# Kernel optimization log

Measured on AMD Instinct MI355X. Metric: run time of the kernel, lower is better.

Reference implementation:

```python
import jax, jax.numpy as jnp
import numpy as np
import math

B, T, N, D = 2, 2048, 16, 128


def setup_inputs() -> dict:
    key = jax.random.key(0)
    ks = jax.random.split(key, 9)
    s = 1.0 / math.sqrt(D)
    return {
        "x": jax.random.normal(ks[0], (B, T, N, D), dtype=jnp.float32),
        "wq": jax.random.normal(ks[1], (D, D), dtype=jnp.float32) * s,
        "bq": jax.random.normal(ks[2], (D,), dtype=jnp.float32) * 0.02,
        "wk": jax.random.normal(ks[3], (D, D), dtype=jnp.float32) * s,
        "bk": jax.random.normal(ks[4], (D,), dtype=jnp.float32) * 0.02,
        "wv": jax.random.normal(ks[5], (D, D), dtype=jnp.float32) * s,
        "bv": jax.random.normal(ks[6], (D,), dtype=jnp.float32) * 0.02,
        "wp": jax.random.normal(ks[7], (D, D), dtype=jnp.float32) * s,
        "bp": jax.random.normal(ks[8], (D,), dtype=jnp.float32) * 0.02,
    }


def reference(x, wq, bq, wk, bk, wv, bv, wp, bp):
    # x: (B, T, N, D); per-head Linear projections (torch y = x @ W.T + b)
    d = x.shape[-1]
    q = jnp.einsum("btnd,ed->btne", x, wq) + bq  # (B,T,N,D)
    k = jnp.einsum("btnd,ed->btne", x, wk) + bk
    v = jnp.einsum("btnd,ed->btne", x, wv) + bv
    scale = 1.0 / jnp.sqrt(jnp.asarray(d, dtype=x.dtype))
    # scores: (B, N, T, T)
    scores = jnp.einsum("btnd,bsnd->bnts", q, k) * scale
    t = scores.shape[-1]
    causal = jnp.tril(jnp.ones((t, t), dtype=bool))  # (T,T)
    scores = jnp.where(causal[None, None], scores, jnp.asarray(-jnp.inf, scores.dtype))
    w = jax.nn.softmax(scores, axis=-1)
    att = jnp.einsum("bnts,bsnd->btnd", w, v)  # (B,T,N,D)
    out = jnp.einsum("btnd,ed->btne", att, wp) + bp
    return out
```

## Files before the change

### kernel.cpp

```cpp
#include <hip/hip_runtime.h>
#include <cmath>

#define BB 2
#define TT 2048
#define NN 16
#define DD 128
#define NROWS (BB*TT*NN)
#define PLANE (TT*DD)
#define KP 132
#define VP 68

typedef unsigned short u16;
typedef unsigned int   u32;
typedef __attribute__((ext_vector_type(8)))  short s8v;
typedef __attribute__((ext_vector_type(16))) float vf16;

__device__ u16 g_Q [(size_t)NROWS * DD];
__device__ u16 g_K [(size_t)NROWS * DD];
__device__ u16 g_V [(size_t)NROWS * DD];
__device__ u16 g_VT[(size_t)NROWS * DD];

__device__ __forceinline__ u16 f2bf(float f) {
    return (u16)((__float_as_uint(f) + 0x8000u) >> 16);
}
__device__ __forceinline__ u32 pk2(float a, float b) {
    return ((__float_as_uint(a) + 0x8000u) >> 16)
         | ((__float_as_uint(b) + 0x8000u) & 0xFFFF0000u);
}
__device__ __forceinline__ void st8(u16* p, const float4& a, const float4& b) {
    uint2 lo, hi;
    lo.x = pk2(a.x, a.y); lo.y = pk2(a.z, a.w);
    hi.x = pk2(b.x, b.y); hi.y = pk2(b.z, b.w);
    *(uint2*)p       = lo;
    *(uint2*)(p + 4) = hi;
}
__device__ __forceinline__ s8v ld8(const u16* p) {
    short4 a = *(const short4*)p;
    short4 b = *(const short4*)(p + 4);
    return (s8v){a.x, a.y, a.z, a.w, b.x, b.y, b.z, b.w};
}

__global__ __launch_bounds__(256)
void qkv_proj_kernel(const float* __restrict__ x,
                     const float* __restrict__ Wq, const float* __restrict__ Bq,
                     const float* __restrict__ Wk, const float* __restrict__ Bk,
                     const float* __restrict__ Wv, const float* __restrict__ Bv)
{
    __shared__ u16 Xs[128*KP];
    __shared__ u16 Ws[128*KP];

    const int t  = threadIdx.x;
    const int r0 = blockIdx.x * 128;
    const float4* xsrc = (const float4*)(x + (size_t)r0*DD);

    #pragma unroll
    for (int it = 0; it < 8; ++it) {
        int i = t + 256*it;
        int e = i >> 4, c8 = i & 15;
        st8(&Xs[e*KP + c8*8], xsrc[2*i], xsrc[2*i + 1]);
    }
    #pragma unroll
    for (int it = 0; it < 8; ++it) {
        int i = t + 256*it;
        int e = i >> 4, c8 = i & 15;
        st8(&Ws[e*KP + c8*8], ((const float4*)Wq)[2*i], ((const float4*)Wq)[2*i + 1]);
    }
    __syncthreads();

    const int w   = t >> 6;
    const int l31 = t & 31;
    const int q2  = (t >> 5) & 1;

    s8v af[8];
    #pragma unroll
    for (int s = 0; s < 8; ++s)
        af[s] = ld8(&Xs[(w*32 + l31)*KP + s*16 + q2*8]);

    #pragma unroll
    for (int wsel = 0; wsel < 3; ++wsel) {
        const float* Bi = (wsel == 0) ? Bq : (wsel == 1) ? Bk : Bv;
        u16*         Ot = (wsel == 0) ? g_Q : (wsel == 1) ? g_K : g_V;

        vf16 acc[4];
        #pragma unroll
        for (int et = 0; et < 4; ++et)
            #pragma unroll
            for (int i = 0; i < 16; ++i) acc[et][i] = 0.f;

        #pragma unroll
        for (int s = 0; s < 8; ++s) {
            #pragma unroll
            for (int et = 0; et < 4; ++et) {
                s8v bf = ld8(&Ws[(et*32 + l31)*KP + s*16 + q2*8]);
                acc[et] = __builtin_amdgcn_mfma_f32_32x32x16_bf16(af[s], bf, acc[et], 0, 0, 0);
            }
        }

        float bb[4];
        #pragma unroll
        for (int et = 0; et < 4; ++et) bb[et] = Bi[et*32 + l31];

        #pragma unroll
        for (int r = 0; r < 16; ++r) {
            int rl = (r & 3) + 8*(r >> 2) + 4*q2;
            int rg = r0 + w*32 + rl;
            int b = rg >> 15, rem = rg & 32767;
            int tt = rem >> 4, n = rem & 15;
            size_t orow = (size_t)((b*NN + n)*TT + tt) * DD;
            #pragma unroll
            for (int et = 0; et < 4; ++et)
                Ot[orow + et*32 + l31] = f2bf(acc[et][r] + bb[et]);
        }

        if (wsel < 2) {
            const float* Wn = (wsel == 0) ? Wk : Wv;
            __syncthreads();
            #pragma unroll
            for (int it = 0; it < 8; ++it) {
                int i = t + 256*it;
                int e = i >> 4, c8 = i & 15;
                st8(&Ws[e*KP + c8*8], ((const float4*)Wn)[2*i], ((const float4*)Wn)[2*i + 1]);
            }
            __syncthreads();
        }
    }
}

__global__ __launch_bounds__(256)
void out_proj_kernel(const float* __restrict__ W, const float* __restrict__ Bi,
                     float* __restrict__ out)
{
    __shared__ u16 Ws[128*KP];

    const int t  = threadIdx.x;
    const int r0 = blockIdx.x * 128;

    #pragma unroll
    for (int it = 0; it < 8; ++it) {
        int i = t + 256*it;
        int e = i >> 4, c8 = i & 15;
        st8(&Ws[e*KP + c8*8], ((const float4*)W)[2*i], ((const float4*)W)[2*i + 1]);
    }

    const int w   = t >> 6;
    const int l31 = t & 31;
    const int q2  = (t >> 5) & 1;

    s8v af[8];
    {
        const u16* src = g_Q + (size_t)(r0 + w*32 + l31)*DD;
        #pragma unroll
        for (int s = 0; s < 8; ++s)
            af[s] = *(const s8v*)&src[s*16 + q2*8];
    }
    __syncthreads();

    vf16 acc[4];
    #pragma unroll
    for (int et = 0; et < 4; ++et)
        #pragma unroll
        for (int i = 0; i < 16; ++i) acc[et][i] = 0.f;

    #pragma unroll
    for (int s = 0; s < 8; ++s) {
        #pragma unroll
        for (int et = 0; et < 4; ++et) {
            s8v bf = ld8(&Ws[(et*32 + l31)*KP + s*16 + q2*8]);
            acc[et] = __builtin_amdgcn_mfma_f32_32x32x16_bf16(af[s], bf, acc[et], 0, 0, 0);
        }
    }

    float bb[4];
    #pragma unroll
    for (int et = 0; et < 4; ++et) bb[et] = Bi[et*32 + l31];

    #pragma unroll
    for (int r = 0; r < 16; ++r) {
        int rl = (r & 3) + 8*(r >> 2) + 4*q2;
        int rg = r0 + w*32 + rl;
        int b = rg >> 15, rem = rg & 32767;
        int n = rem >> 11, tt = rem & 2047;
        size_t orow = (size_t)((b*TT + tt)*NN + n) * DD;
        #pragma unroll
        for (int et = 0; et < 4; ++et)
            out[orow + et*32 + l31] = acc[et][r] + bb[et];
    }
}

__global__ __launch_bounds__(256)
void vtrans_kernel()
{
    const int t   = threadIdx.x;
    const int blk = blockIdx.x;
    const int pl  = blk >> 7;
    const int seg = blk & 127;
    const size_t plane = (size_t)pl * PLANE;
    const int w = t >> 6, lane = t & 63;
    const int d   = (w & 1)*64 + lane;
    const int tt0 = seg*16 + (w >> 1)*8;

    const u16* src = g_V + plane + (size_t)tt0*DD + d;
    u16 e[8];
    #pragma unroll
    for (int i = 0; i < 8; ++i) e[i] = src[(size_t)i*DD];
    uint4 pk;
    pk.x = (u32)e[0] | ((u32)e[1] << 16);
    pk.y = (u32)e[2] | ((u32)e[3] << 16);
    pk.z = (u32)e[4] | ((u32)e[5] << 16);
    pk.w = (u32)e[6] | ((u32)e[7] << 16);
    *(uint4*)&g_VT[plane + (size_t)d*TT + tt0] = pk;
}

__global__ __launch_bounds__(256, 2)
void attn_kernel()
{
    __shared__ u16 Ks[64*KP];
    __shared__ u16 Vt[128*VP];

    const int t   = threadIdx.x;
    const int grp = blockIdx.x >> 5;
    const int bn  = blockIdx.x & 31;
    const int qt  = (grp < 8) ? (15 - grp) : (grp - 8);
    const int q0  = qt * 128;
    const size_t plane = (size_t)bn * PLANE;
    const u16* Kg = g_K  + plane;
    const u16* Vg = g_VT + plane;

    const int w      = t >> 6;
    const int lane   = t & 63;
    const int lane31 = lane & 31;
    const int q2     = lane >> 5;
    const int qband  = q0 + 32*w;
    const int qrow   = qband + lane31;

    s8v qf[8];
    {
        const u16* Qg = g_Q + plane + (size_t)qrow * DD;
        #pragma unroll
        for (int s = 0; s < 8; ++s)
            qf[s] = *(const s8v*)&Qg[s*16 + q2*8];
    }

    vf16 accO[4];
    #pragma unroll
    for (int dt = 0; dt < 4; ++dt)
        #pragma unroll
        for (int i = 0; i < 16; ++i) accO[dt][i] = 0.f;

    float mrow = -INFINITY, lrow = 0.f;
    const float sc2 = 0.08838834764831845f * 1.4426950408889634f;

    const int nkt = 2*qt + 2;

    uint4 pk[4], pv[4];
    #pragma unroll
    for (int c = 0; c < 4; ++c) {
        int j = t + 256*c;
        int kr = j >> 4, kc = j & 15;
        pk[c] = *(const uint4*)&Kg[kr*DD + kc*8];
        int vr = j >> 3, vc = j & 7;
        pv[c] = *(const uint4*)&Vg[(size_t)vr*TT + vc*8];
    }

    for (int kt = 0; kt < nkt; ++kt) {
        const int k0 = kt*64;
        __syncthreads();
        #pragma unroll
        for (int c = 0; c < 4; ++c) {
            int j = t + 256*c;
            int kr = j >> 4, kc = j & 15;
            uint2 a, b;
            a.x = pk[c].x; a.y = pk[c].y; b.x = pk[c].z; b.y = pk[c].w;
            *(uint2*)&Ks[kr*KP + kc*8]     = a;
            *(uint2*)&Ks[kr*KP + kc*8 + 4] = b;
            int vr = j >> 3, vc = j & 7;
            a.x = pv[c].x; a.y = pv[c].y; b.x = pv[c].z; b.y = pv[c].w;
            *(uint2*)&Vt[vr*VP + vc*8]     = a;
            *(uint2*)&Vt[vr*VP + vc*8 + 4] = b;
        }
        __syncthreads();

        if (kt + 1 < nkt) {
            const u16* Kg2 = Kg + (size_t)(k0 + 64)*DD;
            const u16* Vg2 = Vg + (k0 + 64);
            #pragma unroll
            for (int c = 0; c < 4; ++c) {
                int j = t + 256*c;
                int kr = j >> 4, kc = j & 15;
                pk[c] = *(const uint4*)&Kg2[kr*DD + kc*8];
                int vr = j >> 3, vc = j & 7;
                pv[c] = *(const uint4*)&Vg2[(size_t)vr*TT + vc*8];
            }
        }

        if (k0 > qband + 31) continue;

        vf16 accS[2];
        #pragma unroll
        for (int kk = 0; kk < 2; ++kk)
            #pragma unroll
            for (int i = 0; i < 16; ++i) accS[kk][i] = 0.f;
        #pragma unroll
        for (int s = 0; s < 8; ++s) {
            #pragma unroll
            for (int kk = 0; kk < 2; ++kk) {
                s8v a = ld8(&Ks[(kk*32 + lane31)*KP + s*16 + q2*8]);
                accS[kk] = __builtin_amdgcn_mfma_f32_32x32x16_bf16(a, qf[s], accS[kk], 0, 0, 0);
            }
        }

        float p[2][16];
        const bool tail = (k0 + 63 > qband);
        #pragma unroll
        for (int kk = 0; kk < 2; ++kk)
            #pragma unroll
            for (int r = 0; r < 16; ++r) {
                float sv = accS[kk][r] * sc2;
                if (tail) {
                    int keyg = k0 + kk*32 + (r & 3) + 8*(r >> 2) + 4*q2;
                    if (keyg > qrow) sv = -INFINITY;
                }
                p[kk][r] = sv;
            }

        float vmax = -INFINITY;
        #pragma unroll
        for (int kk = 0; kk < 2; ++kk)
            #pragma unroll
            for (int r = 0; r < 16; ++r) vmax = fmaxf(vmax, p[kk][r]);
        vmax = fmaxf(vmax, __shfl_xor(vmax, 32));
        float mold = mrow;
        float mnew = fmaxf(mold, vmax);
        float alpha = __builtin_amdgcn_exp2f(mold - mnew);
        mrow = mnew;
        float ls = 0.f;
        #pragma unroll
        for (int kk = 0; kk < 2; ++kk)
            #pragma unroll
            for (int r = 0; r < 16; ++r) {
                float e = __builtin_amdgcn_exp2f(p[kk][r] - mnew);
                p[kk][r] = e;
                ls += e;
            }
        ls += __shfl_xor(ls, 32);
        lrow = lrow*alpha + ls;

        if (__any(mnew > mold)) {
            float ar[16];
            #pragma unroll
            for (int r = 0; r < 16; ++r)
                ar[r] = __shfl(alpha, (r & 3) + 8*(r >> 2) + 4*q2);
            #pragma unroll
            for (int dt = 0; dt < 4; ++dt)
                #pragma unroll
                for (int r = 0; r < 16; ++r) accO[dt][r] *= ar[r];
        }

        s8v pf[4];
        #pragma unroll
        for (int tau = 0; tau < 4; ++tau) {
            int kk = tau >> 1, rb = (tau & 1)*8;
            s8v v;
            #pragma unroll
            for (int j = 0; j < 8; ++j)
                v[j] = (short)(__float_as_uint(p[kk][rb + j]) >> 16);
            pf[tau] = v;
        }

        #pragma unroll
        for (int dt = 0; dt < 4; ++dt) {
            const u16* vp = &Vt[(dt*32 + lane31)*VP];
            #pragma unroll
            for (int tau = 0; tau < 4; ++tau) {
                const u16* q = vp + 16*tau + 4*q2;
                short4 lo = *(const short4*)q;
                short4 hi = *(const short4*)(q + 8);
                s8v bvv = {lo.x, lo.y, lo.z, lo.w, hi.x, hi.y, hi.z, hi.w};
                accO[dt] = __builtin_amdgcn_mfma_f32_32x32x16_bf16(pf[tau], bvv, accO[dt], 0, 0, 0);
            }
        }
    }

    float inv = 1.0f / lrow;
    #pragma unroll
    for (int r = 0; r < 16; ++r) {
        int rl = (r & 3) + 8*(r >> 2) + 4*q2;
        float ir = __shfl(inv, rl);
        u16* op = g_Q + plane + (size_t)(qband + rl)*DD;
        #pragma unroll
        for (int dt = 0; dt < 4; ++dt)
            op[dt*32 + lane31] = f2bf(accO[dt][r] * ir);
    }
}

extern "C" void kernel_launch(void* const* d_in, const int* in_sizes, int n_in,
                              void* d_out, int out_size, void* d_ws, size_t ws_size,
                              hipStream_t stream)
{
    const float* x  = (const float*)d_in[0];
    const float* wq = (const float*)d_in[1];
    const float* bq = (const float*)d_in[2];
    const float* wk = (const float*)d_in[3];
    const float* bk = (const float*)d_in[4];
    const float* wv = (const float*)d_in[5];
    const float* bv = (const float*)d_in[6];
    const float* wp = (const float*)d_in[7];
    const float* bp = (const float*)d_in[8];
    float* out = (float*)d_out;
    (void)d_ws; (void)ws_size;

    dim3 blk(256);
    qkv_proj_kernel<<<dim3(NROWS/128), blk, 0, stream>>>(
        x, wq, bq, wk, bk, wv, bv);
    vtrans_kernel<<<dim3(BB*NN*128), blk, 0, stream>>>();
    attn_kernel<<<dim3(BB*NN*(TT/128)), blk, 0, stream>>>();
    out_proj_kernel<<<dim3(NROWS/128), blk, 0, stream>>>(wp, bp, out);
}
```

Baseline: 204.9 us.

## Shrink attention blocks to 64 queries, fold softmax scale into Q, lazy rescale

The attention kernel now uses 128-thread blocks covering 64 query rows, doubling the grid and removing the per-wave skip of masked tiles, with a new causal load-balancing order. The softmax scale and log2e are folded into Q at projection time. The online softmax now rescales only when the running max grows by more than 8, which saves multiplies but risks accumulator range growth. MFMA sections get raised wave priority, and the V transpose goes through shared memory so global reads are coalesced. Each thread also now holds twice as many prefetch registers.

New measurement: 198.9 us. 1.03x faster.

```diff
diff --git a/kernel.cpp b/kernel.cpp
--- a/kernel.cpp
+++ b/kernel.cpp
@@ -108,8 +108,11 @@
             int tt = rem >> 4, n = rem & 15;
             size_t orow = (size_t)((b*NN + n)*TT + tt) * DD;
             #pragma unroll
-            for (int et = 0; et < 4; ++et)
-                Ot[orow + et*32 + l31] = f2bf(acc[et][r] + bb[et]);
+            for (int et = 0; et < 4; ++et) {
+                float ov = acc[et][r] + bb[et];
+                if (wsel == 0) ov *= 0.12752053685940512f;
+                Ot[orow + et*32 + l31] = f2bf(ov);
+            }
         }
 
         if (wsel < 2) {
@@ -190,28 +193,39 @@
 __global__ __launch_bounds__(256)
 void vtrans_kernel()
 {
+    __shared__ u16 L[64*KP];
+
     const int t   = threadIdx.x;
     const int blk = blockIdx.x;
-    const int pl  = blk >> 7;
-    const int seg = blk & 127;
+    const int pl  = blk >> 5;
+    const int tt0 = (blk & 31) * 64;
     const size_t plane = (size_t)pl * PLANE;
-    const int w = t >> 6, lane = t & 63;
-    const int d   = (w & 1)*64 + lane;
-    const int tt0 = seg*16 + (w >> 1)*8;
-
-    const u16* src = g_V + plane + (size_t)tt0*DD + d;
-    u16 e[8];
-    #pragma unroll
-    for (int i = 0; i < 8; ++i) e[i] = src[(size_t)i*DD];
-    uint4 pk;
-    pk.x = (u32)e[0] | ((u32)e[1] << 16);
-    pk.y = (u32)e[2] | ((u32)e[3] << 16);
-    pk.z = (u32)e[4] | ((u32)e[5] << 16);
-    pk.w = (u32)e[6] | ((u32)e[7] << 16);
-    *(uint4*)&g_VT[plane + (size_t)d*TT + tt0] = pk;
-}
-
-__global__ __launch_bounds__(256, 2)
+
+    #pragma unroll
+    for (int c = 0; c < 4; ++c) {
+        int j = t + 256*c;
+        int row = j >> 4, c16 = j & 15;
+        uint4 v = *(const uint4*)&g_V[plane + (size_t)(tt0 + row)*DD + c16*8];
+        *(uint4*)&L[row*KP + c16*8] = v;
+    }
+    __syncthreads();
+    #pragma unroll
+    for (int c = 0; c < 4; ++c) {
+        int j = t + 256*c;
+        int d = j >> 3, tc = j & 7;
+        u16 e[8];
+        #pragma unroll
+        for (int i = 0; i < 8; ++i) e[i] = L[(tc*8 + i)*KP + d];
+        uint4 pkv;
+        pkv.x = (u32)e[0] | ((u32)e[1] << 16);
+        pkv.y = (u32)e[2] | ((u32)e[3] << 16);
+        pkv.z = (u32)e[4] | ((u32)e[5] << 16);
+        pkv.w = (u32)e[6] | ((u32)e[7] << 16);
+        *(uint4*)&g_VT[plane + (size_t)d*TT + tt0 + tc*8] = pkv;
+    }
+}
+
+__global__ __launch_bounds__(128, 2)
 void attn_kernel()
 {
     __shared__ u16 Ks[64*KP];
@@ -220,8 +234,12 @@
     const int t   = threadIdx.x;
     const int grp = blockIdx.x >> 5;
     const int bn  = blockIdx.x & 31;
-    const int qt  = (grp < 8) ? (15 - grp) : (grp - 8);
-    const int q0  = qt * 128;
+    int qt;
+    if      (grp < 8)  qt = 31 - grp;
+    else if (grp < 16) qt = grp - 8;
+    else if (grp < 24) qt = 39 - grp;
+    else               qt = grp - 16;
+
     const size_t plane = (size_t)bn * PLANE;
     const u16* Kg = g_K  + plane;
     const u16* Vg = g_VT + plane;
@@ -230,7 +248,7 @@
     const int lane   = t & 63;
     const int lane31 = lane & 31;
     const int q2     = lane >> 5;
-    const int qband  = q0 + 32*w;
+    const int qband  = qt*64 + 32*w;
     const int qrow   = qband + lane31;
 
     s8v qf[8];
@@ -248,14 +266,13 @@
         for (int i = 0; i < 16; ++i) accO[dt][i] = 0.f;
 
     float mrow = -INFINITY, lrow = 0.f;
-    const float sc2 = 0.08838834764831845f * 1.4426950408889634f;
-
-    const int nkt = 2*qt + 2;
-
-    uint4 pk[4], pv[4];
-    #pragma unroll
-    for (int c = 0; c < 4; ++c) {
-        int j = t + 256*c;
+
+    const int nkt = qt + 1;
+
+    uint4 pk[8], pv[8];
+    #pragma unroll
+    for (int c = 0; c < 8; ++c) {
+        int j = t + 128*c;
         int kr = j >> 4, kc = j & 15;
         pk[c] = *(const uint4*)&Kg[kr*DD + kc*8];
         int vr = j >> 3, vc = j & 7;
@@ -266,8 +283,8 @@
         const int k0 = kt*64;
         __syncthreads();
         #pragma unroll
-        for (int c = 0; c < 4; ++c) {
-            int j = t + 256*c;
+        for (int c = 0; c < 8; ++c) {
+            int j = t + 128*c;
             int kr = j >> 4, kc = j & 15;
             uint2 a, b;
             a.x = pk[c].x; a.y = pk[c].y; b.x = pk[c].z; b.y = pk[c].w;
@@ -284,8 +301,8 @@
             const u16* Kg2 = Kg + (size_t)(k0 + 64)*DD;
             const u16* Vg2 = Vg + (k0 + 64);
             #pragma unroll
-            for (int c = 0; c < 4; ++c) {
-                int j = t + 256*c;
+            for (int c = 0; c < 8; ++c) {
+                int j = t + 128*c;
                 int kr = j >> 4, kc = j & 15;
                 pk[c] = *(const uint4*)&Kg2[kr*DD + kc*8];
                 int vr = j >> 3, vc = j & 7;
@@ -293,13 +310,12 @@
             }
         }
 
-        if (k0 > qband + 31) continue;
-
         vf16 accS[2];
         #pragma unroll
         for (int kk = 0; kk < 2; ++kk)
             #pragma unroll
             for (int i = 0; i < 16; ++i) accS[kk][i] = 0.f;
+        __builtin_amdgcn_s_setprio(1);
         #pragma unroll
         for (int s = 0; s < 8; ++s) {
             #pragma unroll
@@ -308,14 +324,15 @@
                 accS[kk] = __builtin_amdgcn_mfma_f32_32x32x16_bf16(a, qf[s], accS[kk], 0, 0, 0);
             }
         }
+        __builtin_amdgcn_s_setprio(0);
 
         float p[2][16];
-        const bool tail = (k0 + 63 > qband);
+        const bool tail = (kt == qt);
         #pragma unroll
         for (int kk = 0; kk < 2; ++kk)
             #pragma unroll
             for (int r = 0; r < 16; ++r) {
-                float sv = accS[kk][r] * sc2;
+                float sv = accS[kk][r];
                 if (tail) {
                     int keyg = k0 + kk*32 + (r & 3) + 8*(r >> 2) + 4*q2;
                     if (keyg > qrow) sv = -INFINITY;
@@ -323,29 +340,19 @@
                 p[kk][r] = sv;
             }
 
-        float vmax = -INFINITY;
-        #pragma unroll
-        for (int kk = 0; kk < 2; ++kk)
-            #pragma unroll
-            for (int r = 0; r < 16; ++r) vmax = fmaxf(vmax, p[kk][r]);
+        float v0 = -INFINITY, v1 = -INFINITY;
+        #pragma unroll
+        for (int r = 0; r < 16; ++r) {
+            v0 = fmaxf(v0, p[0][r]);
+            v1 = fmaxf(v1, p[1][r]);
+        }
+        float vmax = fmaxf(v0, v1);
         vmax = fmaxf(vmax, __shfl_xor(vmax, 32));
-        float mold = mrow;
-        float mnew = fmaxf(mold, vmax);
-        float alpha = __builtin_amdgcn_exp2f(mold - mnew);
-        mrow = mnew;
-        float ls = 0.f;
-        #pragma unroll
-        for (int kk = 0; kk < 2; ++kk)
-            #pragma unroll
-            for (int r = 0; r < 16; ++r) {
-                float e = __builtin_amdgcn_exp2f(p[kk][r] - mnew);
-                p[kk][r] = e;
-                ls += e;
-            }
-        ls += __shfl_xor(ls, 32);
-        lrow = lrow*alpha + ls;
-
-        if (__any(mnew > mold)) {
+
+        if (!__all(vmax <= mrow + 8.f)) {
+            float mnew  = fmaxf(mrow, vmax);
+            float alpha = __builtin_amdgcn_exp2f(mrow - mnew);
+            lrow *= alpha;
             float ar[16];
             #pragma unroll
             for (int r = 0; r < 16; ++r)
@@ -354,7 +361,20 @@
             for (int dt = 0; dt < 4; ++dt)
                 #pragma unroll
                 for (int r = 0; r < 16; ++r) accO[dt][r] *= ar[r];
-        }
+            mrow = mnew;
+        }
+
+        float ls0 = 0.f, ls1 = 0.f;
+        #pragma unroll
+        for (int r = 0; r < 16; ++r) {
+            float e0 = __builtin_amdgcn_exp2f(p[0][r] - mrow);
+            float e1 = __builtin_amdgcn_exp2f(p[1][r] - mrow);
+            p[0][r] = e0; p[1][r] = e1;
+            ls0 += e0; ls1 += e1;
+        }
+        float ls = ls0 + ls1;
+        ls += __shfl_xor(ls, 32);
+        lrow += ls;
 
         s8v pf[4];
         #pragma unroll
@@ -367,6 +387,7 @@
             pf[tau] = v;
         }
 
+        __builtin_amdgcn_s_setprio(1);
         #pragma unroll
         for (int dt = 0; dt < 4; ++dt) {
             const u16* vp = &Vt[(dt*32 + lane31)*VP];
@@ -379,6 +400,7 @@
                 accO[dt] = __builtin_amdgcn_mfma_f32_32x32x16_bf16(pf[tau], bvv, accO[dt], 0, 0, 0);
             }
         }
+        __builtin_amdgcn_s_setprio(0);
     }
 
     float inv = 1.0f / lrow;
@@ -409,10 +431,9 @@
     float* out = (float*)d_out;
     (void)d_ws; (void)ws_size;
 
-    dim3 blk(256);
-    qkv_proj_kernel<<<dim3(NROWS/128), blk, 0, stream>>>(
+    qkv_proj_kernel<<<dim3(NROWS/128), dim3(256), 0, stream>>>(
         x, wq, bq, wk, bk, wv, bv);
-    vtrans_kernel<<<dim3(BB*NN*128), blk, 0, stream>>>();
-    attn_kernel<<<dim3(BB*NN*(TT/128)), blk, 0, stream>>>();
-    out_proj_kernel<<<dim3(NROWS/128), blk, 0, stream>>>(wp, bp, out);
-}
+    vtrans_kernel<<<dim3(BB*NN*(TT/64)), dim3(256), 0, stream>>>();
+    attn_kernel<<<dim3(BB*NN*(TT/64)), dim3(128), 0, stream>>>();
+    out_proj_kernel<<<dim3(NROWS/128), dim3(256), 0, stream>>>(wp, bp, out);
+}
```
